# Optimization experiments

Hardware: AMD Instinct MI355X
Metric: run time of the kernel (lower is better)

## Reference

```python
import jax, jax.numpy as jnp
import numpy as np

N = 8192
EARTH_R = 6371.0      # km
MAX_DIST = 300.0      # max_distance_km
THRESHOLD = 0.3


def setup_inputs() -> dict:
    key = jax.random.key(0)
    k1, k2, k3, k4 = jax.random.split(key, 4)
    lat = 25.0 + 25.0 * jax.random.uniform(k1, (N,), dtype=jnp.float32)    # 25..50 N
    lon = -125.0 + 60.0 * jax.random.uniform(k2, (N,), dtype=jnp.float32)  # -125..-65 E
    positions = jnp.stack([lat, lon], axis=1)                              # [N, 2]
    wind_speed = 15.0 * jax.random.uniform(k3, (N,), dtype=jnp.float32)    # 0..15 m/s
    wind_direction = 360.0 * jax.random.uniform(k4, (N,), dtype=jnp.float32)
    return {"positions": positions, "wind_speed": wind_speed, "wind_direction": wind_direction}


def reference(positions, wind_speed, wind_direction):
    # Dense, vectorized equivalent of the original O(N^2) scalar loop.
    # Returns the dense influence matrix (edge weights, zero where no edge)
    # and the boolean edge mask; edge_index = nonzero(mask) off-device.
    lat = jnp.radians(positions[:, 0])
    lon = jnp.radians(positions[:, 1])
    lat1, lat2 = lat[:, None], lat[None, :]          # i = source row, j = target col
    dlat = lat2 - lat1                                # [N, N]
    dlon = lon[None, :] - lon[:, None]

    # Haversine distance (km)
    a = jnp.sin(dlat / 2) ** 2 + jnp.cos(lat1) * jnp.cos(lat2) * jnp.sin(dlon / 2) ** 2
    a = jnp.clip(a, 1e-12, 1.0 - 1e-12)  # avoid sqrt(0)/sqrt(<0) issues on diagonal
    dist = 2.0 * EARTH_R * jnp.arctan2(jnp.sqrt(a), jnp.sqrt(1.0 - a))

    # Bearing from i to j (degrees in [0, 360))
    x = jnp.sin(dlon) * jnp.cos(lat2)
    y = jnp.cos(lat1) * jnp.sin(lat2) - jnp.sin(lat1) * jnp.cos(lat2) * jnp.cos(dlon)
    eye = jnp.eye(positions.shape[0], dtype=bool)
    x = jnp.where(eye, 0.0, x)  # guard atan2(0,0) on diagonal (masked out anyway)
    y = jnp.where(eye, 1.0, y)
    bearing = (jnp.degrees(jnp.arctan2(x, y)) + 360.0) % 360.0

    # Wind/bearing alignment and influence score
    angle_diff = jnp.abs((bearing - wind_direction[:, None] + 180.0) % 360.0 - 180.0)
    alignment = jnp.cos(jnp.radians(angle_diff))
    influence = alignment * (wind_speed[:, None] / 10.0) * jnp.exp(-dist / 100.0)

    mask = (~eye) & (dist <= MAX_DIST) & (influence > THRESHOLD)
    edge_attr_dense = jnp.where(mask, influence, 0.0)  # [N, N]
    return edge_attr_dense, mask
```

## Files before the change

kernel.cpp:

```cpp
#include <hip/hip_runtime.h>
#include <math.h>


#define NN 8192
#define TI 16
#define TJ 1024
#define TAB_FLOATS (NN * 12)

typedef float f4v __attribute__((ext_vector_type(4)));

__global__ __launch_bounds__(256) void precomp_kernel(
    const float* __restrict__ pos,
    const float* __restrict__ wspd,
    const float* __restrict__ wdir,
    float* __restrict__ tab)
{
    const int i = blockIdx.x * 256 + threadIdx.x;
    if (i >= NN) return;
    const float DEG2RAD = 0.017453292519943295f;
    float latr = pos[2 * i]     * DEG2RAD;
    float lonr = pos[2 * i + 1] * DEG2RAD;
    float wr   = wdir[i]        * DEG2RAD;
    float s, c, hs, hc, hsl, hcl, sl, cl, swr, cwr;
    sincosf(latr,        &s,   &c);
    sincosf(0.5f * latr, &hs,  &hc);
    sincosf(0.5f * lonr, &hsl, &hcl);
    sincosf(lonr,        &sl,  &cl);
    sincosf(wr,          &swr, &cwr);
    float* p = tab + i * 12;
    p[0] = s;   p[1] = c;   p[2]  = hs;  p[3]  = hc;
    p[4] = hsl; p[5] = hcl; p[6]  = sl;  p[7]  = cl;
    p[8] = swr; p[9] = cwr; p[10] = wspd[i] / 10.0f; p[11] = 0.0f;
}

__device__ __forceinline__ void pair_body(
    float is, float ic, float ihs, float ihc,
    float ihsl, float ihcl, float isl, float icl,
    float swr, float cwr, float ws10,
    float js, float jc, float jhs, float jhc,
    float jhsl, float jhcl, float jsl, float jcl,
    bool offdiag, float* ev, float* mv)
{
    float shlat = jhs * ihc - jhc * ihs;
    float shlon = jhsl * ihcl - jhcl * ihsl;
    float cc = ic * jc;
    float a = shlat * shlat + cc * (shlon * shlon);
    float ac = fminf(fmaxf(a, 1e-12f), 1.0f);

    float s = sqrtf(ac);
    float s2 = s * s;
    float dist = fmaf(s * s2, 2123.6667f, s * 12742.0f);

    float sdlon = jsl * icl - jcl * isl;
    float cdlon = jcl * icl + jsl * isl;
    float x = sdlon * jc;
    float y = ic * js - (is * jc) * cdlon;

    float num = y * cwr + x * swr;
    float h2  = x * x + y * y;
    float align = num * rsqrtf(h2);

    float infl = align * ws10 * __expf(dist * -0.01f);
    bool m = offdiag && (dist <= 300.0f) && (infl > 0.3f);
    *ev = m ? infl : 0.0f;
    *mv = m ? 1.0f : 0.0f;
}

__global__ __launch_bounds__(256) void dyn_graph_tab_kernel(
    const float* __restrict__ tab,
    float* __restrict__ out)
{
    __shared__ __align__(16) float irow[TI * 12];

    const int tid   = threadIdx.x;
    const int i0    = blockIdx.y * TI;
    const int jbase = blockIdx.x * TJ + tid * 4;

    if (tid < TI * 3) {
        ((float4*)irow)[tid] = ((const float4*)tab)[i0 * 3 + tid];
    }

    float js[4], jc[4], jhs[4], jhc[4], jhsl[4], jhcl[4], jsl[4], jcl[4];
    #pragma unroll
    for (int k = 0; k < 4; ++k) {
        const float4* q = (const float4*)tab + (size_t)(jbase + k) * 3;
        float4 A = q[0], B = q[1];
        js[k]   = A.x; jc[k]   = A.y; jhs[k] = A.z; jhc[k] = A.w;
        jhsl[k] = B.x; jhcl[k] = B.y; jsl[k] = B.z; jcl[k] = B.w;
    }

    __syncthreads();

    #pragma unroll 1
    for (int r = 0; r < TI; ++r) {
        const float4* p4 = (const float4*)&irow[r * 12];
        float4 A = p4[0], B = p4[1], C = p4[2];
        const int i = i0 + r;

        f4v ev, mv;
        #pragma unroll
        for (int k = 0; k < 4; ++k) {
            float e, m;
            pair_body(A.x, A.y, A.z, A.w, B.x, B.y, B.z, B.w, C.x, C.y, C.z,
                      js[k], jc[k], jhs[k], jhc[k], jhsl[k], jhcl[k], jsl[k], jcl[k],
                      (jbase + k) != i, &e, &m);
            ev[k] = e; mv[k] = m;
        }

        size_t idx = (size_t)i * NN + jbase;
        __builtin_nontemporal_store(ev, (f4v*)(out + idx));
        __builtin_nontemporal_store(mv, (f4v*)(out + (size_t)NN * NN + idx));
    }
}

__global__ __launch_bounds__(256) void dyn_graph_kernel_fb(
    const float* __restrict__ pos,
    const float* __restrict__ wspd,
    const float* __restrict__ wdir,
    float* __restrict__ out)
{
    __shared__ __align__(16) float irow[TI * 12];
    const int tid   = threadIdx.x;
    const int i0    = blockIdx.y * TI;
    const int jbase = blockIdx.x * TJ + tid * 4;
    const float DEG2RAD = 0.017453292519943295f;

    if (tid < TI) {
        int i = i0 + tid;
        float latr = pos[2 * i]     * DEG2RAD;
        float lonr = pos[2 * i + 1] * DEG2RAD;
        float wr   = wdir[i]        * DEG2RAD;
        float s, c, hs, hc, hsl, hcl, sl, cl, swr, cwr;
        sincosf(latr,        &s,   &c);
        sincosf(0.5f * latr, &hs,  &hc);
        sincosf(0.5f * lonr, &hsl, &hcl);
        sincosf(lonr,        &sl,  &cl);
        sincosf(wr,          &swr, &cwr);
        float* p = &irow[tid * 12];
        p[0] = s;   p[1] = c;   p[2]  = hs;  p[3]  = hc;
        p[4] = hsl; p[5] = hcl; p[6]  = sl;  p[7]  = cl;
        p[8] = swr; p[9] = cwr; p[10] = wspd[i] / 10.0f; p[11] = 0.0f;
    }

    float4 p01 = *(const float4*)(pos + 2 * jbase);
    float4 p23 = *(const float4*)(pos + 2 * jbase + 4);
    float jlat[4] = { p01.x, p01.z, p23.x, p23.z };
    float jlon[4] = { p01.y, p01.w, p23.y, p23.w };
    float js[4], jc[4], jhs[4], jhc[4], jhsl[4], jhcl[4], jsl[4], jcl[4];
    #pragma unroll
    for (int k = 0; k < 4; ++k) {
        float latr = jlat[k] * DEG2RAD;
        float lonr = jlon[k] * DEG2RAD;
        sincosf(latr,        &js[k],   &jc[k]);
        sincosf(0.5f * latr, &jhs[k],  &jhc[k]);
        sincosf(0.5f * lonr, &jhsl[k], &jhcl[k]);
        sincosf(lonr,        &jsl[k],  &jcl[k]);
    }
    __syncthreads();

    #pragma unroll 1
    for (int r = 0; r < TI; ++r) {
        const float4* p4 = (const float4*)&irow[r * 12];
        float4 A = p4[0], B = p4[1], C = p4[2];
        const int i = i0 + r;
        f4v ev, mv;
        #pragma unroll
        for (int k = 0; k < 4; ++k) {
            float e, m;
            pair_body(A.x, A.y, A.z, A.w, B.x, B.y, B.z, B.w, C.x, C.y, C.z,
                      js[k], jc[k], jhs[k], jhc[k], jhsl[k], jhcl[k], jsl[k], jcl[k],
                      (jbase + k) != i, &e, &m);
            ev[k] = e; mv[k] = m;
        }
        size_t idx = (size_t)i * NN + jbase;
        __builtin_nontemporal_store(ev, (f4v*)(out + idx));
        __builtin_nontemporal_store(mv, (f4v*)(out + (size_t)NN * NN + idx));
    }
}

extern "C" void kernel_launch(void* const* d_in, const int* in_sizes, int n_in,
                              void* d_out, int out_size, void* d_ws, size_t ws_size,
                              hipStream_t stream) {
    const float* pos  = (const float*)d_in[0];
    const float* wspd = (const float*)d_in[1];
    const float* wdir = (const float*)d_in[2];
    float* out = (float*)d_out;

    dim3 grid(NN / TJ, NN / TI);
    dim3 block(256);

    if (ws_size >= (size_t)TAB_FLOATS * sizeof(float)) {
        float* tab = (float*)d_ws;
        precomp_kernel<<<dim3(NN / 256), block, 0, stream>>>(pos, wspd, wdir, tab);
        dyn_graph_tab_kernel<<<grid, block, 0, stream>>>(tab, out);
    } else {
        dyn_graph_kernel_fb<<<grid, block, 0, stream>>>(pos, wspd, wdir, out);
    }
}
```

Baseline: 540.9 us.

## Switch to one-block-per-row kernel with compact j-table and deferred mask stores

Replaces the 16-row by 1024-column tiled kernel with a kernel where each block handles one full output row, re-reading a packed 8-float j-table from cache for every row instead of keeping j values in registers across 16 rows. The mask bits are accumulated in a register and the mask row is written after all influence stores, so the two output streams are written in separate phases rather than interleaved. The aim is to make the write pattern per block more sequential and to shrink per-thread register state. In exchange, j-table traffic rises about 16x because the data is no longer reused across rows, and the grid grows to 8192 blocks.

```diff
diff --git a/kernel.cpp b/kernel.cpp
--- a/kernel.cpp
+++ b/kernel.cpp
@@ -3,9 +3,10 @@
 
 
 #define NN 8192
-#define TI 16
-#define TJ 1024
-#define TAB_FLOATS (NN * 12)
+#define TI_FB 16
+#define TJ_FB 1024
+#define TABI_FLOATS (NN * 12)
+#define TABJ_FLOATS (NN * 8)
 
 typedef float f4v __attribute__((ext_vector_type(4)));
 
@@ -13,7 +14,8 @@
     const float* __restrict__ pos,
     const float* __restrict__ wspd,
     const float* __restrict__ wdir,
-    float* __restrict__ tab)
+    float* __restrict__ tab_i,
+    float* __restrict__ tab_j)
 {
     const int i = blockIdx.x * 256 + threadIdx.x;
     if (i >= NN) return;
@@ -27,10 +29,13 @@
     sincosf(0.5f * lonr, &hsl, &hcl);
     sincosf(lonr,        &sl,  &cl);
     sincosf(wr,          &swr, &cwr);
-    float* p = tab + i * 12;
+    float* p = tab_i + i * 12;
     p[0] = s;   p[1] = c;   p[2]  = hs;  p[3]  = hc;
     p[4] = hsl; p[5] = hcl; p[6]  = sl;  p[7]  = cl;
     p[8] = swr; p[9] = cwr; p[10] = wspd[i] / 10.0f; p[11] = 0.0f;
+    float* q = tab_j + i * 8;
+    q[0] = s;   q[1] = c;   q[2] = hs;  q[3] = hc;
+    q[4] = hsl; q[5] = hcl; q[6] = sl;  q[7] = cl;
 }
 
 __device__ __forceinline__ void pair_body(
@@ -39,7 +44,7 @@
     float swr, float cwr, float ws10,
     float js, float jc, float jhs, float jhc,
     float jhsl, float jhcl, float jsl, float jcl,
-    bool offdiag, float* ev, float* mv)
+    bool offdiag, float* ev, bool* mout)
 {
     float shlat = jhs * ihc - jhc * ihs;
     float shlon = jhsl * ihcl - jhcl * ihsl;
@@ -63,53 +68,55 @@
     float infl = align * ws10 * __expf(dist * -0.01f);
     bool m = offdiag && (dist <= 300.0f) && (infl > 0.3f);
     *ev = m ? infl : 0.0f;
-    *mv = m ? 1.0f : 0.0f;
-}
-
-__global__ __launch_bounds__(256) void dyn_graph_tab_kernel(
-    const float* __restrict__ tab,
+    *mout = m;
+}
+
+__global__ __launch_bounds__(256) void row_kernel(
+    const float* __restrict__ tab_i,
+    const float* __restrict__ tab_j,
     float* __restrict__ out)
 {
-    __shared__ __align__(16) float irow[TI * 12];
-
-    const int tid   = threadIdx.x;
-    const int i0    = blockIdx.y * TI;
-    const int jbase = blockIdx.x * TJ + tid * 4;
-
-    if (tid < TI * 3) {
-        ((float4*)irow)[tid] = ((const float4*)tab)[i0 * 3 + tid];
-    }
-
-    float js[4], jc[4], jhs[4], jhc[4], jhsl[4], jhcl[4], jsl[4], jcl[4];
-    #pragma unroll
-    for (int k = 0; k < 4; ++k) {
-        const float4* q = (const float4*)tab + (size_t)(jbase + k) * 3;
-        float4 A = q[0], B = q[1];
-        js[k]   = A.x; jc[k]   = A.y; jhs[k] = A.z; jhc[k] = A.w;
-        jhsl[k] = B.x; jhcl[k] = B.y; jsl[k] = B.z; jcl[k] = B.w;
-    }
-
-    __syncthreads();
+    const int i   = blockIdx.x;
+    const int tid = threadIdx.x;
+
+    const float* pi = tab_i + i * 12;
+    const float is  = pi[0], ic  = pi[1], ihs = pi[2], ihc = pi[3];
+    const float ihsl= pi[4], ihcl= pi[5], isl = pi[6], icl = pi[7];
+    const float swr = pi[8], cwr = pi[9], ws10= pi[10];
+
+    const size_t row = (size_t)i * NN;
+    unsigned maskbits = 0;
 
     #pragma unroll 1
-    for (int r = 0; r < TI; ++r) {
-        const float4* p4 = (const float4*)&irow[r * 12];
-        float4 A = p4[0], B = p4[1], C = p4[2];
-        const int i = i0 + r;
-
-        f4v ev, mv;
+    for (int jc4 = 0; jc4 < 8; ++jc4) {
+        const int jbase = jc4 * 1024 + tid * 4;
+
+        f4v ev;
+        unsigned mb = 0;
         #pragma unroll
         for (int k = 0; k < 4; ++k) {
-            float e, m;
-            pair_body(A.x, A.y, A.z, A.w, B.x, B.y, B.z, B.w, C.x, C.y, C.z,
-                      js[k], jc[k], jhs[k], jhc[k], jhsl[k], jhcl[k], jsl[k], jcl[k],
+            const float4* q = (const float4*)tab_j + (size_t)(jbase + k) * 2;
+            float4 A = q[0], B = q[1];
+            float e; bool m;
+            pair_body(is, ic, ihs, ihc, ihsl, ihcl, isl, icl, swr, cwr, ws10,
+                      A.x, A.y, A.z, A.w, B.x, B.y, B.z, B.w,
                       (jbase + k) != i, &e, &m);
-            ev[k] = e; mv[k] = m;
+            ev[k] = e;
+            mb |= (m ? 1u : 0u) << k;
         }
 
-        size_t idx = (size_t)i * NN + jbase;
-        __builtin_nontemporal_store(ev, (f4v*)(out + idx));
-        __builtin_nontemporal_store(mv, (f4v*)(out + (size_t)NN * NN + idx));
+        __builtin_nontemporal_store(ev, (f4v*)(out + row + jbase));
+        maskbits |= mb << (jc4 * 4);
+    }
+
+    float* mrow = out + (size_t)NN * NN + row;
+    #pragma unroll
+    for (int jc4 = 0; jc4 < 8; ++jc4) {
+        f4v mv;
+        #pragma unroll
+        for (int k = 0; k < 4; ++k)
+            mv[k] = ((maskbits >> (jc4 * 4 + k)) & 1u) ? 1.0f : 0.0f;
+        __builtin_nontemporal_store(mv, (f4v*)(mrow + jc4 * 1024 + tid * 4));
     }
 }
 
@@ -119,13 +126,13 @@
     const float* __restrict__ wdir,
     float* __restrict__ out)
 {
-    __shared__ __align__(16) float irow[TI * 12];
+    __shared__ __align__(16) float irow[TI_FB * 12];
     const int tid   = threadIdx.x;
-    const int i0    = blockIdx.y * TI;
-    const int jbase = blockIdx.x * TJ + tid * 4;
+    const int i0    = blockIdx.y * TI_FB;
+    const int jbase = blockIdx.x * TJ_FB + tid * 4;
     const float DEG2RAD = 0.017453292519943295f;
 
-    if (tid < TI) {
+    if (tid < TI_FB) {
         int i = i0 + tid;
         float latr = pos[2 * i]     * DEG2RAD;
         float lonr = pos[2 * i + 1] * DEG2RAD;
@@ -146,12 +153,12 @@
     float4 p23 = *(const float4*)(pos + 2 * jbase + 4);
     float jlat[4] = { p01.x, p01.z, p23.x, p23.z };
     float jlon[4] = { p01.y, p01.w, p23.y, p23.w };
-    float js[4], jc[4], jhs[4], jhc[4], jhsl[4], jhcl[4], jsl[4], jcl[4];
+    float js[4], jcv[4], jhs[4], jhc[4], jhsl[4], jhcl[4], jsl[4], jcl[4];
     #pragma unroll
     for (int k = 0; k < 4; ++k) {
         float latr = jlat[k] * DEG2RAD;
         float lonr = jlon[k] * DEG2RAD;
-        sincosf(latr,        &js[k],   &jc[k]);
+        sincosf(latr,        &js[k],   &jcv[k]);
         sincosf(0.5f * latr, &jhs[k],  &jhc[k]);
         sincosf(0.5f * lonr, &jhsl[k], &jhcl[k]);
         sincosf(lonr,        &jsl[k],  &jcl[k]);
@@ -159,18 +166,18 @@
     __syncthreads();
 
     #pragma unroll 1
-    for (int r = 0; r < TI; ++r) {
+    for (int r = 0; r < TI_FB; ++r) {
         const float4* p4 = (const float4*)&irow[r * 12];
         float4 A = p4[0], B = p4[1], C = p4[2];
         const int i = i0 + r;
         f4v ev, mv;
         #pragma unroll
         for (int k = 0; k < 4; ++k) {
-            float e, m;
+            float e; bool m;
             pair_body(A.x, A.y, A.z, A.w, B.x, B.y, B.z, B.w, C.x, C.y, C.z,
-                      js[k], jc[k], jhs[k], jhc[k], jhsl[k], jhcl[k], jsl[k], jcl[k],
+                      js[k], jcv[k], jhs[k], jhc[k], jhsl[k], jhcl[k], jsl[k], jcl[k],
                       (jbase + k) != i, &e, &m);
-            ev[k] = e; mv[k] = m;
+            ev[k] = e; mv[k] = m ? 1.0f : 0.0f;
         }
         size_t idx = (size_t)i * NN + jbase;
         __builtin_nontemporal_store(ev, (f4v*)(out + idx));
@@ -186,14 +193,13 @@
     const float* wdir = (const float*)d_in[2];
     float* out = (float*)d_out;
 
-    dim3 grid(NN / TJ, NN / TI);
-    dim3 block(256);
-
-    if (ws_size >= (size_t)TAB_FLOATS * sizeof(float)) {
-        float* tab = (float*)d_ws;
-        precomp_kernel<<<dim3(NN / 256), block, 0, stream>>>(pos, wspd, wdir, tab);
-        dyn_graph_tab_kernel<<<grid, block, 0, stream>>>(tab, out);
+    if (ws_size >= (size_t)(TABI_FLOATS + TABJ_FLOATS) * sizeof(float)) {
+        float* tab_i = (float*)d_ws;
+        float* tab_j = tab_i + TABI_FLOATS;
+        precomp_kernel<<<dim3(NN / 256), dim3(256), 0, stream>>>(pos, wspd, wdir, tab_i, tab_j);
+        row_kernel<<<dim3(NN), dim3(256), 0, stream>>>(tab_i, tab_j, out);
     } else {
-        dyn_graph_kernel_fb<<<grid, block, 0, stream>>>(pos, wspd, wdir, out);
-    }
-}
+        dim3 grid(NN / TJ_FB, NN / TI_FB);
+        dyn_graph_kernel_fb<<<grid, dim3(256), 0, stream>>>(pos, wspd, wdir, out);
+    }
+}
```

Result: slower. 678.5 us (+25.4%).
